# Kernel tuning notes

Measured on AMD Instinct MI355X. Metric: run time of the kernel, lower is better.

The kernel has to match this reference:

```python
import math
import jax, jax.numpy as jnp
import numpy as np
from jax import lax

CELL = 8
BINS = 9


def setup_inputs() -> dict:
    key = jax.random.key(0)
    x = jax.random.uniform(key, (64, 3, 224, 224), dtype=jnp.float32)
    return {"x": x}


def reference(x):
    N, C, H, W = x.shape
    # Fixed Sobel buffers: one output channel summing over all input channels.
    sob = jnp.array([[-1.0, 0.0, 1.0], [-2.0, 0.0, 2.0], [-1.0, 0.0, 1.0]], dtype=x.dtype)
    kx = jnp.broadcast_to(sob, (1, C, 3, 3))          # SobelX weight [O=1, I=C, 3, 3]
    ky = jnp.broadcast_to(sob.T, (1, C, 3, 3))        # SobelY weight
    dn = ('NCHW', 'OIHW', 'NCHW')
    gx = lax.conv_general_dilated(x, kx, (1, 1), 'SAME', dimension_numbers=dn)  # [N,1,H,W]
    gy = lax.conv_general_dilated(x, ky, (1, 1), 'SAME', dimension_numbers=dn)
    mag = jnp.sqrt(gx * gx + gy * gy)                 # [N,1,H,W]
    ang = jnp.abs(jnp.arctan2(gx, gy))                # unsigned gradients -> [0, pi]
    bin_idx = jnp.floor(ang / math.pi * (BINS - 1)).astype(jnp.int32)  # [N,1,H,W], values in [0, BINS-1]
    # scatter_(1, bin_idx, mag) == one-hot along bin axis times magnitude
    onehot = (bin_idx == jnp.arange(BINS, dtype=jnp.int32)[None, :, None, None]).astype(x.dtype)  # [N,BINS,H,W]
    vol = onehot * mag                                # broadcast over bin axis
    # AvgPool2d(cell) * cell^2 == per-cell sum
    hog = vol.reshape(N, BINS, H // CELL, CELL, W // CELL, CELL).sum(axis=(3, 5))  # [N,BINS,H/8,W/8]
    return hog.reshape(N, -1)
```

## Files before the change

kernel.cpp:

```cpp
#include <hip/hip_runtime.h>
#include <math.h>


namespace {
constexpr int Himg = 224;
constexpr int Wimg = 224;
constexpr int NCELL = 28;
constexpr int BINS  = 9;
constexpr int ROWS  = 10;
constexpr int LDSW  = 232;
constexpr int NCHUNK = ROWS * 56;

__global__ __launch_bounds__(256, 6) void hog_kernel(const float* __restrict__ x,
                                                     float* __restrict__ out) {
    const int n  = blockIdx.y;
    const int cr = blockIdx.x;
    const int t  = threadIdx.x;

    __shared__ float s[ROWS][LDSW];

    if (t < ROWS * 8) {
        int r = t >> 3;
        int c = t & 7;
        int col = (c < 4) ? c : (224 + c);
        s[r][col] = 0.0f;
    }

    const int h0 = cr * 8 - 1;
    const float* xb = x + (size_t)n * 3 * Himg * Wimg;

    float4 va[3];
    int    lofs[3];
    bool   act[3];
#pragma unroll
    for (int k = 0; k < 3; ++k) {
        int idx = t + 256 * k;
        bool pred = (k < 2) || (idx < NCHUNK);
        int r = pred ? (idx / 56) : 0;
        int q = idx - r * 56;
        int w = q * 4;
        int h = h0 + r;
        act[k]  = pred;
        lofs[k] = r * LDSW + 4 + w;
        float4 v = make_float4(0.f, 0.f, 0.f, 0.f);
        if (pred && h >= 0 && h < Himg) {
            const float* r0 = xb + (size_t)h * Wimg + w;
            float4 a  = *(const float4*)(r0);
            float4 b  = *(const float4*)(r0 + Himg * Wimg);
            float4 c4 = *(const float4*)(r0 + 2 * Himg * Wimg);
            v.x = a.x + b.x + c4.x;
            v.y = a.y + b.y + c4.y;
            v.z = a.z + b.z + c4.z;
            v.w = a.w + b.w + c4.w;
        }
        va[k] = v;
    }
#pragma unroll
    for (int k = 0; k < 3; ++k)
        if (act[k]) *(float4*)&((float*)s)[lofs[k]] = va[k];
    __syncthreads();

    const float PI_F = 3.14159265358979323846f;
    const float CK[8] = {0.92387953f, 0.70710678f, 0.38268343f, 0.0f,
                         -0.38268343f, -0.70710678f, -0.92387953f, -1.0f};

    if (t < 224) {
        const int w = t;
        float ml = s[0][3 + w], mc = s[0][4 + w], mr = s[0][5 + w];
        float zl = s[1][3 + w], zc = s[1][4 + w], zr = s[1][5 + w];
        float acc[BINS];
#pragma unroll
        for (int j = 0; j < BINS; ++j) acc[j] = 0.0f;

#pragma unroll
        for (int i = 0; i < 8; ++i) {
            float pl = s[i + 2][3 + w];
            float pc = s[i + 2][4 + w];
            float pr = s[i + 2][5 + w];

            float gx = (mr - ml) + 2.0f * (zr - zl) + (pr - pl);
            float gy = (pl + 2.0f * pc + pr) - (ml + 2.0f * mc + mr);
            float mag = sqrtf(gx * gx + gy * gy);

            float negy = -gy;
            int bin = 0;
            float guard = 1e30f;
#pragma unroll
            for (int j = 0; j < 8; ++j) {
                float sj = fmaf(mag, CK[j], negy);
                bin += (sj >= 0.0f) ? 1 : 0;
                guard = fminf(guard, fabsf(sj));
            }
            if (guard < mag * 1e-4f) {
                float ang = fabsf(atan2f(gx, gy));
                bin = (int)(ang / PI_F * 8.0f);
                bin = bin > 8 ? 8 : bin;
            }
#pragma unroll
            for (int j = 0; j < BINS; ++j) acc[j] += (bin == j) ? mag : 0.0f;

            ml = zl; mc = zc; mr = zr;
            zl = pl; zc = pc; zr = pr;
        }

#pragma unroll
        for (int j = 0; j < BINS; ++j) {
            float v = acc[j];
            v += __shfl_down(v, 4);
            v += __shfl_down(v, 2);
            v += __shfl_down(v, 1);
            acc[j] = v;
        }
        if ((w & 7) == 0) {
            const int cw = w >> 3;
#pragma unroll
            for (int j = 0; j < BINS; ++j)
                out[((size_t)n * BINS + j) * (NCELL * NCELL) + (size_t)cr * NCELL + cw] = acc[j];
        }
    }
}
}

extern "C" void kernel_launch(void* const* d_in, const int* in_sizes, int n_in,
                              void* d_out, int out_size, void* d_ws, size_t ws_size,
                              hipStream_t stream) {
    const float* x = (const float*)d_in[0];
    float* out = (float*)d_out;
    const int N = in_sizes[0] / (3 * Himg * Wimg);
    dim3 grid(NCELL, N);
    hog_kernel<<<grid, 256, 0, stream>>>(x, out);
}
```

Baseline: 83.89 us.

## Process two cell rows per block and accumulate cumulative bin counts

```diff
diff --git a/kernel.cpp b/kernel.cpp
--- a/kernel.cpp
+++ b/kernel.cpp
@@ -7,14 +7,14 @@
 constexpr int Wimg = 224;
 constexpr int NCELL = 28;
 constexpr int BINS  = 9;
-constexpr int ROWS  = 10;
+constexpr int ROWS  = 18;
 constexpr int LDSW  = 232;
 constexpr int NCHUNK = ROWS * 56;
 
-__global__ __launch_bounds__(256, 6) void hog_kernel(const float* __restrict__ x,
-                                                     float* __restrict__ out) {
+__global__ __launch_bounds__(256) void hog_kernel(const float* __restrict__ x,
+                                                  float* __restrict__ out) {
     const int n  = blockIdx.y;
-    const int cr = blockIdx.x;
+    const int pr = blockIdx.x;
     const int t  = threadIdx.x;
 
     __shared__ float s[ROWS][LDSW];
@@ -26,16 +26,16 @@
         s[r][col] = 0.0f;
     }
 
-    const int h0 = cr * 8 - 1;
+    const int h0 = pr * 16 - 1;
     const float* xb = x + (size_t)n * 3 * Himg * Wimg;
 
-    float4 va[3];
-    int    lofs[3];
-    bool   act[3];
+    float4 va[4];
+    int    lofs[4];
+    bool   act[4];
 #pragma unroll
-    for (int k = 0; k < 3; ++k) {
+    for (int k = 0; k < 4; ++k) {
         int idx = t + 256 * k;
-        bool pred = (k < 2) || (idx < NCHUNK);
+        bool pred = (k < 3) || (idx < NCHUNK);
         int r = pred ? (idx / 56) : 0;
         int q = idx - r * 56;
         int w = q * 4;
@@ -56,7 +56,7 @@
         va[k] = v;
     }
 #pragma unroll
-    for (int k = 0; k < 3; ++k)
+    for (int k = 0; k < 4; ++k)
         if (act[k]) *(float4*)&((float*)s)[lofs[k]] = va[k];
     __syncthreads();
 
@@ -73,49 +73,65 @@
         for (int j = 0; j < BINS; ++j) acc[j] = 0.0f;
 
 #pragma unroll
-        for (int i = 0; i < 8; ++i) {
-            float pl = s[i + 2][3 + w];
-            float pc = s[i + 2][4 + w];
-            float pr = s[i + 2][5 + w];
+        for (int half = 0; half < 2; ++half) {
+#pragma unroll
+            for (int i = 0; i < 8; ++i) {
+                const int rr = half * 8 + i + 2;
+                float pl = s[rr][3 + w];
+                float pc = s[rr][4 + w];
+                float pr2 = s[rr][5 + w];
 
-            float gx = (mr - ml) + 2.0f * (zr - zl) + (pr - pl);
-            float gy = (pl + 2.0f * pc + pr) - (ml + 2.0f * mc + mr);
-            float mag = sqrtf(gx * gx + gy * gy);
+                float gx = (mr - ml) + 2.0f * (zr - zl) + (pr2 - pl);
+                float gy = (pl + 2.0f * pc + pr2) - (ml + 2.0f * mc + mr);
+                float mag = sqrtf(gx * gx + gy * gy);
 
-            float negy = -gy;
-            int bin = 0;
-            float guard = 1e30f;
+                float negy = -gy;
+                float guard = 1e30f;
+                float mge[8];
 #pragma unroll
-            for (int j = 0; j < 8; ++j) {
-                float sj = fmaf(mag, CK[j], negy);
-                bin += (sj >= 0.0f) ? 1 : 0;
-                guard = fminf(guard, fabsf(sj));
+                for (int j = 0; j < 8; ++j) {
+                    float sj = fmaf(mag, CK[j], negy);
+                    mge[j] = (sj >= 0.0f) ? mag : 0.0f;
+                    guard = fminf(guard, fabsf(sj));
+                }
+                if (guard < mag * 1e-4f) {
+                    float ang = fabsf(atan2f(gx, gy));
+                    int bin = (int)(ang / PI_F * 8.0f);
+                    bin = bin > 8 ? 8 : bin;
+#pragma unroll
+                    for (int j = 0; j < 8; ++j)
+                        mge[j] = (bin >= j + 1) ? mag : 0.0f;
+                }
+                acc[0] += mag;
+#pragma unroll
+                for (int j = 0; j < 8; ++j) acc[j + 1] += mge[j];
+
+                ml = zl; mc = zc; mr = zr;
+                zl = pl; zc = pc; zr = pr2;
             }
-            if (guard < mag * 1e-4f) {
-                float ang = fabsf(atan2f(gx, gy));
-                bin = (int)(ang / PI_F * 8.0f);
-                bin = bin > 8 ? 8 : bin;
+
+            float red[BINS];
+#pragma unroll
+            for (int j = 0; j < BINS; ++j) {
+                float v = acc[j];
+                v += __shfl_down(v, 4);
+                v += __shfl_down(v, 2);
+                v += __shfl_down(v, 1);
+                red[j] = v;
             }
+            if ((w & 7) == 0) {
+                const int cw = w >> 3;
+                const int cr = pr * 2 + half;
 #pragma unroll
-            for (int j = 0; j < BINS; ++j) acc[j] += (bin == j) ? mag : 0.0f;
-
-            ml = zl; mc = zc; mr = zr;
-            zl = pl; zc = pc; zr = pr;
-        }
-
+                for (int j = 0; j < BINS; ++j) {
+                    float hv = (j < 8) ? (red[j] - red[j + 1]) : red[8];
+                    out[((size_t)n * BINS + j) * (NCELL * NCELL) + (size_t)cr * NCELL + cw] = hv;
+                }
+            }
+            if (half == 0) {
 #pragma unroll
-        for (int j = 0; j < BINS; ++j) {
-            float v = acc[j];
-            v += __shfl_down(v, 4);
-            v += __shfl_down(v, 2);
-            v += __shfl_down(v, 1);
-            acc[j] = v;
-        }
-        if ((w & 7) == 0) {
-            const int cw = w >> 3;
-#pragma unroll
-            for (int j = 0; j < BINS; ++j)
-                out[((size_t)n * BINS + j) * (NCELL * NCELL) + (size_t)cr * NCELL + cw] = acc[j];
+                for (int j = 0; j < BINS; ++j) acc[j] = 0.0f;
+            }
         }
     }
 }
@@ -127,6 +143,6 @@
     const float* x = (const float*)d_in[0];
     float* out = (float*)d_out;
     const int N = in_sizes[0] / (3 * Himg * Wimg);
-    dim3 grid(NCELL, N);
+    dim3 grid(NCELL / 2, N);
     hog_kernel<<<grid, 256, 0, stream>>>(x, out);
 }
```

New measurement: 84.27 us. Within noise of the previous version (+0.5%).
